# Performance work log

Measured on AMD Instinct MI355X. Metric: run time of the kernel, lower is better.

Reference implementation:

```python
import jax, jax.numpy as jnp
import numpy as np

B, S, F, H, K, NG = 256, 512, 128, 128, 8, 4
LD = H + 1  # latent_dim
EPS = 1e-12


def _ln(x, w, b):
    u = x.mean(-1, keepdims=True)
    s = ((x - u) ** 2).mean(-1, keepdims=True)
    return w * (x - u) / jnp.sqrt(s + EPS) + b


def _gru_cell(x, h, Wih, Whh, bih, bhh):
    # torch GRU gate order: reset, update, new
    gi = x @ Wih.T + bih
    gh = h @ Whh.T + bhh
    ir, iz, inn = jnp.split(gi, 3, axis=-1)
    hr, hz, hn = jnp.split(gh, 3, axis=-1)
    r = jax.nn.sigmoid(ir + hr)
    z = jax.nn.sigmoid(iz + hz)
    n = jnp.tanh(inn + r * hn)
    return (1.0 - z) * n + z * h


def setup_inputs():
    key = jax.random.key(0)
    ks = jax.random.split(key, 24)
    s = 1.0 / np.sqrt(H)
    d = {}
    d['input_data'] = jax.random.normal(ks[0], (B, S, F), jnp.float32)
    d['enc_Wih'] = jax.random.uniform(ks[1], (3 * H, F), jnp.float32, -s, s)
    d['enc_Whh'] = jax.random.uniform(ks[2], (3 * H, H), jnp.float32, -s, s)
    d['enc_bih'] = jax.random.uniform(ks[3], (3 * H,), jnp.float32, -s, s)
    d['enc_bhh'] = jax.random.uniform(ks[4], (3 * H,), jnp.float32, -s, s)
    d['dec_Wih'] = jax.random.uniform(ks[5], (3 * H, F), jnp.float32, -s, s)
    d['dec_Whh'] = jax.random.uniform(ks[6], (3 * H, H), jnp.float32, -s, s)
    d['dec_bih'] = jax.random.uniform(ks[7], (3 * H,), jnp.float32, -s, s)
    d['dec_bhh'] = jax.random.uniform(ks[8], (3 * H,), jnp.float32, -s, s)
    d['out_W'] = jax.random.uniform(ks[9], (F, H), jnp.float32, -s, s)
    d['out_b'] = jax.random.uniform(ks[10], (F,), jnp.float32, -s, s)
    d['prototypes'] = jax.random.normal(ks[11], (K, H), jnp.float32) * s
    d['lnz_w'] = jnp.ones((H,), jnp.float32)
    d['lnz_b'] = jnp.zeros((H,), jnp.float32)
    d['lnp_w'] = jnp.ones((H,), jnp.float32)
    d['lnp_b'] = jnp.zeros((H,), jnp.float32)
    d['lna_w'] = jnp.ones((H,), jnp.float32)
    d['lna_b'] = jnp.zeros((H,), jnp.float32)
    d['beta_seq'] = jax.random.normal(ks[12], (K, H), jnp.float32) * s
    d['est1_W'] = jax.random.uniform(ks[13], (10, LD), jnp.float32, -1.0 / np.sqrt(LD), 1.0 / np.sqrt(LD))
    d['est1_b'] = jax.random.uniform(ks[14], (10,), jnp.float32, -1.0 / np.sqrt(LD), 1.0 / np.sqrt(LD))
    d['est2_W'] = jax.random.uniform(ks[15], (NG, 10), jnp.float32, -1.0 / np.sqrt(10.0), 1.0 / np.sqrt(10.0))
    d['est2_b'] = jax.random.uniform(ks[16], (NG,), jnp.float32, -1.0 / np.sqrt(10.0), 1.0 / np.sqrt(10.0))
    return d


def reference(input_data, enc_Wih, enc_Whh, enc_bih, enc_bhh,
              dec_Wih, dec_Whh, dec_bih, dec_bhh, out_W, out_b,
              prototypes, lnz_w, lnz_b, lnp_w, lnp_b, lna_w, lna_b,
              beta_seq, est1_W, est1_b, est2_W, est2_b):
    bsz = input_data.shape[0]
    x_t = jnp.swapaxes(input_data, 0, 1)  # [S,B,F]

    def enc_step(h, x):
        return _gru_cell(x, h, enc_Wih, enc_Whh, enc_bih, enc_bhh), None

    h0 = jnp.zeros((bsz, H), input_data.dtype)
    h_enc, _ = jax.lax.scan(enc_step, h0, x_t)  # final hidden [B,H]

    # eval-mode decoder: emit output from hidden, then feed output back in,
    # iterating over time indices i = S-1 .. 0
    def dec_step(h, _):
        o = h @ out_W.T + out_b
        hn = _gru_cell(o, h, dec_Wih, dec_Whh, dec_bih, dec_bhh)
        return hn, o

    _, outs = jax.lax.scan(dec_step, h_enc, None, length=S)  # [S,B,F] in reversed time
    output = jnp.swapaxes(outs, 0, 1)[:, ::-1, :]  # [B,S,F]

    a = input_data.reshape(bsz, -1)
    bb = output.reshape(bsz, -1)
    na = jnp.maximum(jnp.linalg.norm(a, axis=1), 1e-8)
    nb = jnp.maximum(jnp.linalg.norm(bb, axis=1), 1e-8)
    rec_cosine = jnp.sum(a * bb, axis=1) / (na * nb)  # [B]

    # intention clustering: softmax over K prototypes
    z_ln = _ln(h_enc, lnz_w, lnz_b)            # [B,H]
    prot_ln = _ln(prototypes, lnp_w, lnp_b)    # [K,H]
    attn = jax.nn.softmax((z_ln @ prot_ln.T) / np.sqrt(H), axis=-1)  # [B,K]

    # intention aggregation: outer product [B,K,1]x[B,1,H]
    dis = beta_seq[None, :, :] + attn[:, :, None] * h_enc[:, None, :]  # [B,K,H]
    dis = _ln(dis, lna_w, lna_b)

    # resample rows per column: independent batch permutation per category
    perm_keys = jax.random.split(jax.random.key(42), K)
    perms = jnp.stack([jax.random.permutation(perm_keys[k], bsz) for k in range(K)], axis=1)  # [B,K]
    dis_perm = jnp.take_along_axis(dis, perms[:, :, None], axis=0)

    z = jnp.concatenate([dis.mean(axis=1), rec_cosine[:, None]], axis=1)  # [B,LD]
    h1 = jnp.tanh(z @ est1_W.T + est1_b)  # dropout is identity in eval
    gamma = jax.nn.softmax(h1 @ est2_W.T + est2_b, axis=1)
    return (h_enc, output, z, gamma, dis, dis_perm)
```

## Files before the change

### kernel.cpp

```cpp
#include <hip/hip_runtime.h>
#include <stdint.h>

#define Bsz 256
#define Ssz 512
#define Fsz 128
#define Hsz 128

#define HOFF_OUT   32768
#define HOFF_Z     16809984
#define HOFF_G     16843008
#define HOFF_DIS   16844032
#define HOFF_DISP  17106176

typedef __attribute__((ext_vector_type(8))) short short8;
typedef __attribute__((ext_vector_type(4))) short short4_;
typedef __attribute__((ext_vector_type(4))) float f32x4;

__device__ __forceinline__ short f2bf(float f){
  uint32_t u = __float_as_uint(f);
  u += 0x7FFFu + ((u >> 16) & 1u);
  return (short)(u >> 16);
}
__device__ __forceinline__ float bf2f(short h){
  return __uint_as_float(((uint32_t)(uint16_t)h) << 16);
}

__device__ __forceinline__ f32x4 MFMA(short8 a, short8 b, f32x4 c){
  f32x4 d;
  asm("v_mfma_f32_16x16x32_bf16 %0, %1, %2, %3" : "=v"(d) : "v"(a), "v"(b), "v"(c));
  return d;
}

__device__ __forceinline__ short8 ldcvt8(const float* p){
  float4 a = *(const float4*)p;
  float4 b = *(const float4*)(p + 4);
  short8 v;
  v[0]=f2bf(a.x); v[1]=f2bf(a.y); v[2]=f2bf(a.z); v[3]=f2bf(a.w);
  v[4]=f2bf(b.x); v[5]=f2bf(b.y); v[6]=f2bf(b.z); v[7]=f2bf(b.w);
  return v;
}
__device__ __forceinline__ void ldcvt8_2(const float* p, short8& hi, short8& lo){
  #pragma unroll
  for (int q = 0; q < 8; ++q){
    float v = p[q];
    short h = f2bf(v);
    hi[q] = h;
    lo[q] = f2bf(v - bf2f(h));
  }
}

__device__ __forceinline__ float sigm(float x){ return 1.0f/(1.0f + __expf(-x)); }
__device__ __forceinline__ float tanh_(float x){
  x = fminf(15.0f, fmaxf(-15.0f, x));
  float e = __expf(2.0f*x);
  return (e - 1.0f)/(e + 1.0f);
}

__device__ __forceinline__ int swzb(int row, int bo){ return row*256 + (bo ^ ((row & 7) << 4)); }
#define H32IDX(row, j) ((row)*128 + ((j) ^ ((((row) >> 2) & 3) << 3)))

__device__ __forceinline__ short8 ldfrag(const short* buf, int l15, int lg, int kt){
  return *(const short8*)((const char*)buf + swzb(l15, (kt*32 + lg*8)*2));
}

__device__ __forceinline__ float rsum32(float v){
  v += __shfl_xor(v,1); v += __shfl_xor(v,2); v += __shfl_xor(v,4);
  v += __shfl_xor(v,8); v += __shfl_xor(v,16); return v;
}
__device__ __forceinline__ float rsum16(float v){
  v += __shfl_xor(v,1); v += __shfl_xor(v,2); v += __shfl_xor(v,4); v += __shfl_xor(v,8);
  return v;
}

__device__ __forceinline__ void tf2x32(uint32_t k0, uint32_t k1, uint32_t x0, uint32_t x1,
                                       uint32_t& o0, uint32_t& o1){
  const uint32_t ks2 = k0 ^ k1 ^ 0x1BD11BDAu;
  uint32_t a = x0 + k0, b = x1 + k1;
#define RR(r) { a += b; b = (b << r) | (b >> (32 - r)); b ^= a; }
  RR(13) RR(15) RR(26) RR(6)   a += k1;  b += ks2 + 1u;
  RR(17) RR(29) RR(16) RR(24)  a += ks2; b += k0 + 2u;
  RR(13) RR(15) RR(26) RR(6)   a += k0;  b += k1 + 3u;
  RR(17) RR(29) RR(16) RR(24)  a += k1;  b += ks2 + 4u;
  RR(13) RR(15) RR(26) RR(6)   a += ks2; b += k0 + 5u;
#undef RR
  o0 = a; o1 = b;
}

__global__ void perm_kernel(int* __restrict__ perm){
  const int k = blockIdx.x;
  const int tid = threadIdx.x;
  __shared__ unsigned long long ck[256];
  __shared__ int nv[256];
  uint32_t pk0, pk1, sub0, sub1, o0, o1;
  tf2x32(0u, 42u, 0u, (uint32_t)k, pk0, pk1);
  tf2x32(pk0, pk1, 0u, 1u, sub0, sub1);
  tf2x32(sub0, sub1, 0u, (uint32_t)tid, o0, o1);
  const uint32_t sk = o0 ^ o1;
  unsigned long long ci = (((unsigned long long)sk) << 32) | (unsigned)tid;
  ck[tid] = ci;
  __syncthreads();
  int rank = 0;
  #pragma unroll 8
  for (int jj = 0; jj < 256; ++jj) rank += (ck[jj] < ci) ? 1 : 0;
  nv[rank] = tid;
  __syncthreads();
  perm[tid*8 + k] = nv[tid];
}

__global__ void mprep(const float* __restrict__ dWih, const float* __restrict__ dWhh,
                      const float* __restrict__ oW, const float* __restrict__ oB,
                      const float* __restrict__ dBih,
                      float* __restrict__ M, float* __restrict__ c){
  const int r = blockIdx.x;
  const int kk = threadIdx.x;
  float acc = 0.f;
  for (int f = 0; f < 128; ++f) acc += dWih[r*128 + f] * oW[f*128 + kk];
  if (r < 256) acc += dWhh[r*128 + kk];
  M[r*128 + kk] = acc;
  if (kk == 0){
    float cc = dBih[r];
    for (int f = 0; f < 128; ++f) cc += dWih[r*128 + f] * oB[f];
    c[r] = cc;
  }
}

__global__ void gatherk(const float* __restrict__ out_dis, float* __restrict__ out_disp,
                        const int* __restrict__ perm){
  int idx = blockIdx.x*512 + threadIdx.x;
  int jj = idx & 127, kk = (idx >> 7) & 7, b = idx >> 10;
  out_disp[idx] = out_dis[(perm[b*8 + kk]*8 + kk)*128 + jj];
}

__global__ __launch_bounds__(512, 2) void seqae_main(
    const float* __restrict__ x_in,
    const float* __restrict__ eWih, const float* __restrict__ eWhh,
    const float* __restrict__ eBih, const float* __restrict__ eBhh,
    const float* __restrict__ dWhh, const float* __restrict__ dBhh,
    const float* __restrict__ oW, const float* __restrict__ oB,
    const float* __restrict__ prot,
    const float* __restrict__ lnzW, const float* __restrict__ lnzB,
    const float* __restrict__ lnpW, const float* __restrict__ lnpB,
    const float* __restrict__ lnaW, const float* __restrict__ lnaB,
    const float* __restrict__ beta,
    const float* __restrict__ e1W, const float* __restrict__ e1B,
    const float* __restrict__ e2W, const float* __restrict__ e2B,
    const float* __restrict__ Mws, const float* __restrict__ cws,
    float* __restrict__ out)
{
  __shared__ short hbuf[2][2048];
  __shared__ short hlob[2][2048];
  __shared__ short xbuf[2][2048];
  __shared__ float h32[2][2048];
  __shared__ float henc[2048];

  const int tid = threadIdx.x;
  const int w = tid >> 6, lane = tid & 63;
  const int l15 = lane & 15, lg = lane >> 4;
  const int bbase = blockIdx.x * 16;
  const int jrow = w*16 + l15;
  const int srow = tid >> 5, schunk = tid & 31;
  const int j = jrow;

  const float be_r  = eBih[j]       + eBhh[j];
  const float be_z  = eBih[128 + j] + eBhh[128 + j];
  const float be_in = eBih[256 + j];
  const float be_hn = eBhh[256 + j];
  const float bd_r  = cws[j]        + dBhh[j];
  const float bd_z  = cws[128 + j]  + dBhh[128 + j];
  const float bd_in = cws[256 + j];
  const float bd_hn = dBhh[256 + j];
  const float b_o   = oB[j];

  for (int i = tid; i < 2048; i += 512){ h32[0][i] = 0.f; hbuf[0][i] = 0; hlob[0][i] = 0; }

  short8 ex_r[4], ex_z[4], ex_i[4];
  short8 eh_rh[4], eh_rl[4], eh_zh[4], eh_zl[4], eh_nh[4], eh_nl[4];
  #pragma unroll
  for (int kt = 0; kt < 4; ++kt){
    const int off = kt*32 + lg*8;
    ex_r[kt] = ldcvt8(eWih + (      j)*128 + off);
    ex_z[kt] = ldcvt8(eWih + (128 + j)*128 + off);
    ex_i[kt] = ldcvt8(eWih + (256 + j)*128 + off);
    ldcvt8_2(eWhh + (      j)*128 + off, eh_rh[kt], eh_rl[kt]);
    ldcvt8_2(eWhh + (128 + j)*128 + off, eh_zh[kt], eh_zl[kt]);
    ldcvt8_2(eWhh + (256 + j)*128 + off, eh_nh[kt], eh_nl[kt]);
  }

  float na_reg = 0.f;
  {
    float4 xf = *(const float4*)(x_in + ((bbase + srow)*Ssz + 0)*Fsz + schunk*4);
    na_reg += xf.x*xf.x + xf.y*xf.y + xf.z*xf.z + xf.w*xf.w;
    short4_ s; s[0]=f2bf(xf.x); s[1]=f2bf(xf.y); s[2]=f2bf(xf.z); s[3]=f2bf(xf.w);
    *(short4_*)((char*)&xbuf[0][0] + swzb(srow, schunk*8)) = s;
  }
  __syncthreads();

  for (int t = 0; t < Ssz; ++t){
    const int cur = t & 1, nxt = cur ^ 1;
    float4 xf;
    const bool hav = (t + 1 < Ssz);
    if (hav) xf = *(const float4*)(x_in + ((bbase + srow)*Ssz + (t+1))*Fsz + schunk*4);

    short8 axf[4], ahh[4], ahl[4];
    #pragma unroll
    for (int kt = 0; kt < 4; ++kt){
      axf[kt] = ldfrag(&xbuf[cur][0], l15, lg, kt);
      ahh[kt] = ldfrag(&hbuf[cur][0], l15, lg, kt);
      ahl[kt] = ldfrag(&hlob[cur][0], l15, lg, kt);
    }
    f32x4 ar = {0,0,0,0}, az = {0,0,0,0}, ai = {0,0,0,0}, an = {0,0,0,0};
    #pragma unroll
    for (int kt = 0; kt < 4; ++kt){
      ar = MFMA(axf[kt], ex_r[kt], ar);
      az = MFMA(axf[kt], ex_z[kt], az);
      ai = MFMA(axf[kt], ex_i[kt], ai);
      ar = MFMA(ahh[kt], eh_rh[kt], ar);
      ar = MFMA(ahl[kt], eh_rh[kt], ar);
      ar = MFMA(ahh[kt], eh_rl[kt], ar);
      az = MFMA(ahh[kt], eh_zh[kt], az);
      az = MFMA(ahl[kt], eh_zh[kt], az);
      az = MFMA(ahh[kt], eh_zl[kt], az);
      an = MFMA(ahh[kt], eh_nh[kt], an);
      an = MFMA(ahl[kt], eh_nh[kt], an);
      an = MFMA(ahh[kt], eh_nl[kt], an);
    }
    #pragma unroll
    for (int reg = 0; reg < 4; ++reg){
      const int row = lg*4 + reg;
      float r = sigm(ar[reg] + be_r);
      float z = sigm(az[reg] + be_z);
      float n = tanh_(ai[reg] + be_in + r*(an[reg] + be_hn));
      float hold = h32[cur][H32IDX(row, j)];
      float hv = n + z*(hold - n);
      h32[nxt][H32IDX(row, j)] = hv;
      short hh = f2bf(hv);
      short hl = f2bf(hv - bf2f(hh));
      *(short*)((char*)&hbuf[nxt][0] + swzb(row, 2*j)) = hh;
      *(short*)((char*)&hlob[nxt][0] + swzb(row, 2*j)) = hl;
    }
    if (hav){
      na_reg += xf.x*xf.x + xf.y*xf.y + xf.z*xf.z + xf.w*xf.w;
      short4_ s; s[0]=f2bf(xf.x); s[1]=f2bf(xf.y); s[2]=f2bf(xf.z); s[3]=f2bf(xf.w);
      *(short4_*)((char*)&xbuf[nxt][0] + swzb(srow, schunk*8)) = s;
    }
    __syncthreads();
  }

  for (int i2 = tid; i2 < 2048; i2 += 512){
    int row = i2 >> 7, jj = i2 & 127;
    float v = h32[0][H32IDX(row, jj)];
    henc[i2] = v;
    out[(bbase + row)*128 + jj] = v;
  }

  short8 d_oh[4], d_ol[4], d_rh[4], d_rl[4], d_zh[4], d_zl[4], d_ih[4], d_il[4], d_nh[4], d_nl[4];
  #pragma unroll
  for (int kt = 0; kt < 4; ++kt){
    const int off = kt*32 + lg*8;
    ldcvt8_2(oW   + (      j)*128 + off, d_oh[kt], d_ol[kt]);
    ldcvt8_2(Mws  + (      j)*128 + off, d_rh[kt], d_rl[kt]);
    ldcvt8_2(Mws  + (128 + j)*128 + off, d_zh[kt], d_zl[kt]);
    ldcvt8_2(Mws  + (256 + j)*128 + off, d_ih[kt], d_il[kt]);
    ldcvt8_2(dWhh + (256 + j)*128 + off, d_nh[kt], d_nl[kt]);
  }

  float dot_p[4] = {0,0,0,0}, nb_p[4] = {0,0,0,0};
  for (int i = 0; i < Ssz; ++i){
    const int cur = i & 1, nxt = cur ^ 1;
    const int tt = Ssz - 1 - i;
    float xv[4];
    #pragma unroll
    for (int reg = 0; reg < 4; ++reg){
      const int row = lg*4 + reg;
      xv[reg] = x_in[((bbase + row)*Ssz + tt)*Fsz + j];
    }
    short8 ahh[4], ahl[4];
    #pragma unroll
    for (int kt = 0; kt < 4; ++kt){
      ahh[kt] = ldfrag(&hbuf[cur][0], l15, lg, kt);
      ahl[kt] = ldfrag(&hlob[cur][0], l15, lg, kt);
    }
    f32x4 ao = {0,0,0,0}, ar = {0,0,0,0}, az = {0,0,0,0}, ai = {0,0,0,0}, an = {0,0,0,0};
    #pragma unroll
    for (int kt = 0; kt < 4; ++kt){
      ao = MFMA(ahh[kt], d_oh[kt], ao);
      ao = MFMA(ahl[kt], d_oh[kt], ao);
      ao = MFMA(ahh[kt], d_ol[kt], ao);
      ar = MFMA(ahh[kt], d_rh[kt], ar);
      ar = MFMA(ahl[kt], d_rh[kt], ar);
      ar = MFMA(ahh[kt], d_rl[kt], ar);
      az = MFMA(ahh[kt], d_zh[kt], az);
      az = MFMA(ahl[kt], d_zh[kt], az);
      az = MFMA(ahh[kt], d_zl[kt], az);
      ai = MFMA(ahh[kt], d_ih[kt], ai);
      ai = MFMA(ahl[kt], d_ih[kt], ai);
      ai = MFMA(ahh[kt], d_il[kt], ai);
      an = MFMA(ahh[kt], d_nh[kt], an);
      an = MFMA(ahl[kt], d_nh[kt], an);
      an = MFMA(ahh[kt], d_nl[kt], an);
    }
    #pragma unroll
    for (int reg = 0; reg < 4; ++reg){
      const int row = lg*4 + reg;
      float o = ao[reg] + b_o;
      float r = sigm(ar[reg] + bd_r);
      float z = sigm(az[reg] + bd_z);
      float n = tanh_(ai[reg] + bd_in + r*(an[reg] + bd_hn));
      float hold = h32[cur][H32IDX(row, j)];
      float hv = n + z*(hold - n);
      h32[nxt][H32IDX(row, j)] = hv;
      short hh = f2bf(hv);
      short hl = f2bf(hv - bf2f(hh));
      *(short*)((char*)&hbuf[nxt][0] + swzb(row, 2*j)) = hh;
      *(short*)((char*)&hlob[nxt][0] + swzb(row, 2*j)) = hl;
      out[HOFF_OUT + ((bbase + row)*Ssz + tt)*Fsz + j] = o;
      dot_p[reg] += xv[reg]*o;
      nb_p[reg]  += o*o;
    }
    __syncthreads();
  }

  float (*s_zln)[128] = reinterpret_cast<float(*)[128]>(&xbuf[0][0]);
  float (*s_pln)[128] = reinterpret_cast<float(*)[128]>(&h32[0][0]);
  float (*s_att)[8]   = reinterpret_cast<float(*)[8]>(&h32[0][1024]);
  float (*s_h1)[10]   = reinterpret_cast<float(*)[10]>(&h32[0][1152]);
  float (*red)[8][16] = reinterpret_cast<float(*)[8][16]>(&h32[1][0]);
  float *s_na = &h32[1][256];
  float *s_rc = &h32[1][272];

  {
    float v = rsum32(na_reg);
    if ((tid & 31) == 0) s_na[srow] = v;
  }
  #pragma unroll
  for (int reg = 0; reg < 4; ++reg){
    float d  = rsum16(dot_p[reg]);
    float nb = rsum16(nb_p[reg]);
    if (l15 == 0){ red[0][w][lg*4 + reg] = d; red[1][w][lg*4 + reg] = nb; }
  }
  __syncthreads();
  if (tid < 16){
    float d = 0.f, nb = 0.f;
    #pragma unroll
    for (int ww = 0; ww < 8; ++ww){ d += red[0][ww][tid]; nb += red[1][ww][tid]; }
    s_rc[tid] = d / (fmaxf(sqrtf(s_na[tid]), 1e-8f) * fmaxf(sqrtf(nb), 1e-8f));
  }

  {
    const int rr = srow, tl = schunk;
    float xv4[4]; float sm = 0.f, sq = 0.f;
    #pragma unroll
    for (int q = 0; q < 4; ++q){ float v = henc[rr*128 + q*32 + tl]; xv4[q] = v; sm += v; sq += v*v; }
    sm = rsum32(sm); sq = rsum32(sq);
    float u = sm*(1.f/128.f), var = sq*(1.f/128.f) - u*u;
    float inv = rsqrtf(var + 1e-12f);
    #pragma unroll
    for (int q = 0; q < 4; ++q){ int jj = q*32 + tl; s_zln[rr][jj] = lnzW[jj]*(xv4[q]-u)*inv + lnzB[jj]; }
  }
  if (tid < 256){
    const int pr = tid >> 5, tl = tid & 31;
    float xv4[4]; float sm = 0.f, sq = 0.f;
    #pragma unroll
    for (int q = 0; q < 4; ++q){ float v = prot[pr*128 + q*32 + tl]; xv4[q] = v; sm += v; sq += v*v; }
    sm = rsum32(sm); sq = rsum32(sq);
    float u = sm*(1.f/128.f), var = sq*(1.f/128.f) - u*u;
    float inv = rsqrtf(var + 1e-12f);
    #pragma unroll
    for (int q = 0; q < 4; ++q){ int jj = q*32 + tl; s_pln[pr][jj] = lnpW[jj]*(xv4[q]-u)*inv + lnpB[jj]; }
  }
  __syncthreads();

  {
    const int gid = tid >> 2, tq = tid & 3;
    const int rr2 = gid >> 3, kk = gid & 7;
    float p = 0.f;
    #pragma unroll 8
    for (int q = 0; q < 32; ++q){ int jj = tq + 4*q; p += s_zln[rr2][jj]*s_pln[kk][jj]; }
    p += __shfl_xor(p, 1); p += __shfl_xor(p, 2);
    if (tq == 0) s_att[rr2][kk] = p * 0.08838834764831845f;
  }
  __syncthreads();
  if (tid < 16){
    float mx = -1e30f;
    #pragma unroll
    for (int kk = 0; kk < 8; ++kk) mx = fmaxf(mx, s_att[tid][kk]);
    float sum = 0.f; float e[8];
    #pragma unroll
    for (int kk = 0; kk < 8; ++kk){ e[kk] = __expf(s_att[tid][kk] - mx); sum += e[kk]; }
    #pragma unroll
    for (int kk = 0; kk < 8; ++kk) s_att[tid][kk] = e[kk]/sum;
  }
  __syncthreads();

  {
    const int rr = srow, tl = schunk;
    float dmq[4] = {0,0,0,0};
    for (int kk = 0; kk < 8; ++kk){
      float a = s_att[rr][kk];
      float vv[4]; float sm = 0.f, sq = 0.f;
      #pragma unroll
      for (int q = 0; q < 4; ++q){
        int jj = q*32 + tl;
        float v = beta[kk*128 + jj] + a*henc[rr*128 + jj];
        vv[q] = v; sm += v; sq += v*v;
      }
      sm = rsum32(sm); sq = rsum32(sq);
      float u = sm*(1.f/128.f), var = sq*(1.f/128.f) - u*u;
      float inv = rsqrtf(var + 1e-12f);
      #pragma unroll
      for (int q = 0; q < 4; ++q){
        int jj = q*32 + tl;
        float dv = lnaW[jj]*(vv[q]-u)*inv + lnaB[jj];
        out[HOFF_DIS + ((bbase + rr)*8 + kk)*128 + jj] = dv;
        dmq[q] += dv;
      }
    }
    #pragma unroll
    for (int q = 0; q < 4; ++q){
      int jj = q*32 + tl;
      float dm = dmq[q]*0.125f;
      out[HOFF_Z + (bbase + rr)*129 + jj] = dm;
      s_zln[rr][jj] = dm;
    }
    if (tl == 0) out[HOFF_Z + (bbase + rr)*129 + 128] = s_rc[rr];
  }
  __syncthreads();

  if (tid < 160){
    const int rr = tid/10, ii = tid%10;
    float acc = e1B[ii];
    const float* wrow = e1W + ii*129;
    for (int dd = 0; dd < 128; ++dd) acc += wrow[dd]*s_zln[rr][dd];
    acc += wrow[128]*s_rc[rr];
    s_h1[rr][ii] = tanh_(acc);
  }
  __syncthreads();
  if (tid < 16){
    float g[4]; float mx = -1e30f;
    #pragma unroll
    for (int ii = 0; ii < 4; ++ii){
      float a = e2B[ii];
      #pragma unroll
      for (int dd = 0; dd < 10; ++dd) a += e2W[ii*10 + dd]*s_h1[tid][dd];
      g[ii] = a; mx = fmaxf(mx, a);
    }
    float sum = 0.f;
    #pragma unroll
    for (int ii = 0; ii < 4; ++ii){ g[ii] = __expf(g[ii] - mx); sum += g[ii]; }
    #pragma unroll
    for (int ii = 0; ii < 4; ++ii) out[HOFF_G + (bbase + tid)*4 + ii] = g[ii]/sum;
  }
}

extern "C" void kernel_launch(void* const* d_in, const int* in_sizes, int n_in,
                              void* d_out, int out_size, void* d_ws, size_t ws_size,
                              hipStream_t stream){
  (void)in_sizes; (void)n_in; (void)out_size; (void)ws_size;
  const float* x    = (const float*)d_in[0];
  const float* eWih = (const float*)d_in[1];
  const float* eWhh = (const float*)d_in[2];
  const float* eBih = (const float*)d_in[3];
  const float* eBhh = (const float*)d_in[4];
  const float* dWih = (const float*)d_in[5];
  const float* dWhh = (const float*)d_in[6];
  const float* dBih = (const float*)d_in[7];
  const float* dBhh = (const float*)d_in[8];
  const float* oW   = (const float*)d_in[9];
  const float* oB   = (const float*)d_in[10];
  const float* prot = (const float*)d_in[11];
  const float* lnzW = (const float*)d_in[12];
  const float* lnzB = (const float*)d_in[13];
  const float* lnpW = (const float*)d_in[14];
  const float* lnpB = (const float*)d_in[15];
  const float* lnaW = (const float*)d_in[16];
  const float* lnaB = (const float*)d_in[17];
  const float* beta = (const float*)d_in[18];
  const float* e1W  = (const float*)d_in[19];
  const float* e1B  = (const float*)d_in[20];
  const float* e2W  = (const float*)d_in[21];
  const float* e2B  = (const float*)d_in[22];

  float* Mws = (float*)d_ws;
  float* cws = Mws + 384*128;
  int*  perm = (int*)(cws + 384);
  float* out = (float*)d_out;

  hipLaunchKernelGGL(mprep, dim3(384), dim3(128), 0, stream, dWih, dWhh, oW, oB, dBih, Mws, cws);
  hipLaunchKernelGGL(perm_kernel, dim3(8), dim3(256), 0, stream, perm);
  hipLaunchKernelGGL(seqae_main, dim3(16), dim3(512), 0, stream,
      x, eWih, eWhh, eBih, eBhh, dWhh, dBhh, oW, oB, prot,
      lnzW, lnzB, lnpW, lnpB, lnaW, lnaB, beta, e1W, e1B, e2W, e2B, Mws, cws, out);
  hipLaunchKernelGGL(gatherk, dim3(512), dim3(512), 0, stream, out + HOFF_DIS, out + HOFF_DISP, perm);
}
```

Before: 2.124 ms.

## Keep GRU state in registers, split MFMA chains, unroll steps with light barriers

```diff
diff --git a/kernel.cpp b/kernel.cpp
--- a/kernel.cpp
+++ b/kernel.cpp
@@ -13,7 +13,6 @@
 #define HOFF_DISP  17106176
 
 typedef __attribute__((ext_vector_type(8))) short short8;
-typedef __attribute__((ext_vector_type(4))) short short4_;
 typedef __attribute__((ext_vector_type(4))) float f32x4;
 
 __device__ __forceinline__ short f2bf(float f){
@@ -32,11 +31,9 @@
 }
 
 __device__ __forceinline__ short8 ldcvt8(const float* p){
-  float4 a = *(const float4*)p;
-  float4 b = *(const float4*)(p + 4);
   short8 v;
-  v[0]=f2bf(a.x); v[1]=f2bf(a.y); v[2]=f2bf(a.z); v[3]=f2bf(a.w);
-  v[4]=f2bf(b.x); v[5]=f2bf(b.y); v[6]=f2bf(b.z); v[7]=f2bf(b.w);
+  #pragma unroll
+  for (int q = 0; q < 8; ++q) v[q] = f2bf(p[q]);
   return v;
 }
 __device__ __forceinline__ void ldcvt8_2(const float* p, short8& hi, short8& lo){
@@ -56,11 +53,10 @@
   return (e - 1.0f)/(e + 1.0f);
 }
 
-__device__ __forceinline__ int swzb(int row, int bo){ return row*256 + (bo ^ ((row & 7) << 4)); }
-#define H32IDX(row, j) ((row)*128 + ((j) ^ ((((row) >> 2) & 3) << 3)))
-
-__device__ __forceinline__ short8 ldfrag(const short* buf, int l15, int lg, int kt){
-  return *(const short8*)((const char*)buf + swzb(l15, (kt*32 + lg*8)*2));
+__device__ __forceinline__ void lbar(){
+  asm volatile("s_waitcnt lgkmcnt(0)" ::: "memory");
+  __builtin_amdgcn_s_barrier();
+  asm volatile("" ::: "memory");
 }
 
 __device__ __forceinline__ float rsum32(float v){
@@ -130,6 +126,8 @@
   int jj = idx & 127, kk = (idx >> 7) & 7, b = idx >> 10;
   out_disp[idx] = out_dis[(perm[b*8 + kk]*8 + kk)*128 + jj];
 }
+
+#define FRAG(base, off) (*(const short8*)((const char*)(base) + (off)))
 
 __global__ __launch_bounds__(512, 2) void seqae_main(
     const float* __restrict__ x_in,
@@ -147,19 +145,17 @@
     const float* __restrict__ Mws, const float* __restrict__ cws,
     float* __restrict__ out)
 {
-  __shared__ short hbuf[2][2048];
-  __shared__ short hlob[2][2048];
-  __shared__ short xbuf[2][2048];
-  __shared__ float h32[2][2048];
-  __shared__ float henc[2048];
+  __shared__ __align__(16) short hbuf[2][2048];
+  __shared__ __align__(16) short hlob[2][2048];
+  __shared__ __align__(16) short xbuf[2][2048];
+  __shared__ __align__(16) float henc[2048];
 
   const int tid = threadIdx.x;
   const int w = tid >> 6, lane = tid & 63;
   const int l15 = lane & 15, lg = lane >> 4;
   const int bbase = blockIdx.x * 16;
-  const int jrow = w*16 + l15;
+  const int j = w*16 + l15;
   const int srow = tid >> 5, schunk = tid & 31;
-  const int j = jrow;
 
   const float be_r  = eBih[j]       + eBhh[j];
   const float be_z  = eBih[128 + j] + eBhh[128 + j];
@@ -171,7 +167,20 @@
   const float bd_hn = dBhh[256 + j];
   const float b_o   = oB[j];
 
-  for (int i = tid; i < 2048; i += 512){ h32[0][i] = 0.f; hbuf[0][i] = 0; hlob[0][i] = 0; }
+  int fo[4];
+  #pragma unroll
+  for (int kt = 0; kt < 4; ++kt)
+    fo[kt] = l15*256 + ((kt*64 + lg*16) ^ ((l15 & 7) << 4));
+  int wo[4];
+  #pragma unroll
+  for (int reg = 0; reg < 4; ++reg){
+    int row = lg*4 + reg;
+    wo[reg] = row*256 + ((2*j) ^ ((row & 7) << 4));
+  }
+  const int xwo = srow*256 + ((schunk*8) ^ ((srow & 7) << 4));
+
+  for (int i = tid; i < 2048; i += 512){ hbuf[0][i] = 0; hlob[0][i] = 0; }
+  float hold[4] = {0.f, 0.f, 0.f, 0.f};
 
   short8 ex_r[4], ex_z[4], ex_i[4];
   short8 eh_rh[4], eh_rl[4], eh_zh[4], eh_zl[4], eh_nh[4], eh_nl[4];
@@ -186,71 +195,99 @@
     ldcvt8_2(eWhh + (256 + j)*128 + off, eh_nh[kt], eh_nl[kt]);
   }
 
+#define STORE_H(NXT, hv) do { \
+    uint32_t pkh0, pkh1, pkl0, pkl1; \
+    asm("v_cvt_pk_bf16_f32 %0, %1, %2" : "=v"(pkh0) : "v"(hv[0]), "v"(hv[1])); \
+    asm("v_cvt_pk_bf16_f32 %0, %1, %2" : "=v"(pkh1) : "v"(hv[2]), "v"(hv[3])); \
+    float l0 = hv[0] - __uint_as_float(pkh0 << 16); \
+    float l1 = hv[1] - __uint_as_float(pkh0 & 0xffff0000u); \
+    float l2 = hv[2] - __uint_as_float(pkh1 << 16); \
+    float l3 = hv[3] - __uint_as_float(pkh1 & 0xffff0000u); \
+    asm("v_cvt_pk_bf16_f32 %0, %1, %2" : "=v"(pkl0) : "v"(l0), "v"(l1)); \
+    asm("v_cvt_pk_bf16_f32 %0, %1, %2" : "=v"(pkl1) : "v"(l2), "v"(l3)); \
+    char* hbp = (char*)&hbuf[NXT][0]; char* lbp = (char*)&hlob[NXT][0]; \
+    *(short*)(hbp + wo[0]) = (short)(pkh0); \
+    *(short*)(hbp + wo[1]) = (short)(pkh0 >> 16); \
+    *(short*)(hbp + wo[2]) = (short)(pkh1); \
+    *(short*)(hbp + wo[3]) = (short)(pkh1 >> 16); \
+    *(short*)(lbp + wo[0]) = (short)(pkl0); \
+    *(short*)(lbp + wo[1]) = (short)(pkl0 >> 16); \
+    *(short*)(lbp + wo[2]) = (short)(pkl1); \
+    *(short*)(lbp + wo[3]) = (short)(pkl1 >> 16); \
+  } while(0)
+
+#define XSTAGE(NXT, xf) do { \
+    na_reg += xf.x*xf.x + xf.y*xf.y + xf.z*xf.z + xf.w*xf.w; \
+    uint32_t p0, p1; \
+    asm("v_cvt_pk_bf16_f32 %0, %1, %2" : "=v"(p0) : "v"(xf.x), "v"(xf.y)); \
+    asm("v_cvt_pk_bf16_f32 %0, %1, %2" : "=v"(p1) : "v"(xf.z), "v"(xf.w)); \
+    *(uint64_t*)((char*)&xbuf[NXT][0] + xwo) = ((uint64_t)p1 << 32) | p0; \
+  } while(0)
+
+#define ENC_STEP(CUR) do { \
+    short8 axf[4], ahh[4], ahl[4]; \
+    _Pragma("unroll") \
+    for (int kt = 0; kt < 4; ++kt){ \
+      axf[kt] = FRAG(&xbuf[CUR][0], fo[kt]); \
+      ahh[kt] = FRAG(&hbuf[CUR][0], fo[kt]); \
+      ahl[kt] = FRAG(&hlob[CUR][0], fo[kt]); \
+    } \
+    f32x4 arA={0,0,0,0}, arB={0,0,0,0}, azA={0,0,0,0}, azB={0,0,0,0}; \
+    f32x4 anA={0,0,0,0}, anB={0,0,0,0}, ai4={0,0,0,0}; \
+    _Pragma("unroll") \
+    for (int kt = 0; kt < 4; ++kt){ \
+      arA = MFMA(axf[kt], ex_r[kt], arA); \
+      azA = MFMA(axf[kt], ex_z[kt], azA); \
+      anA = MFMA(ahh[kt], eh_nh[kt], anA); \
+      ai4 = MFMA(axf[kt], ex_i[kt], ai4); \
+      arB = MFMA(ahh[kt], eh_rh[kt], arB); \
+      azB = MFMA(ahh[kt], eh_zh[kt], azB); \
+      anB = MFMA(ahl[kt], eh_nh[kt], anB); \
+      arA = MFMA(ahl[kt], eh_rh[kt], arA); \
+      azA = MFMA(ahl[kt], eh_zh[kt], azA); \
+      anA = MFMA(ahh[kt], eh_nl[kt], anA); \
+      arB = MFMA(ahh[kt], eh_rl[kt], arB); \
+      azB = MFMA(ahh[kt], eh_zl[kt], azB); \
+    } \
+    f32x4 arS = arA + arB, azS = azA + azB, anS = anA + anB; \
+    float hv[4]; \
+    _Pragma("unroll") \
+    for (int reg = 0; reg < 4; ++reg){ \
+      float r = sigm(arS[reg] + be_r); \
+      float z = sigm(azS[reg] + be_z); \
+      float n = tanh_(ai4[reg] + be_in + r*(anS[reg] + be_hn)); \
+      float h2 = n + z*(hold[reg] - n); \
+      hold[reg] = h2; hv[reg] = h2; \
+    } \
+    STORE_H(CUR ^ 1, hv); \
+  } while(0)
+
   float na_reg = 0.f;
+  const int xoff_lane = ((bbase + srow)*Ssz)*Fsz + schunk*4;
   {
-    float4 xf = *(const float4*)(x_in + ((bbase + srow)*Ssz + 0)*Fsz + schunk*4);
-    na_reg += xf.x*xf.x + xf.y*xf.y + xf.z*xf.z + xf.w*xf.w;
-    short4_ s; s[0]=f2bf(xf.x); s[1]=f2bf(xf.y); s[2]=f2bf(xf.z); s[3]=f2bf(xf.w);
-    *(short4_*)((char*)&xbuf[0][0] + swzb(srow, schunk*8)) = s;
-  }
-  __syncthreads();
-
-  for (int t = 0; t < Ssz; ++t){
-    const int cur = t & 1, nxt = cur ^ 1;
-    float4 xf;
-    const bool hav = (t + 1 < Ssz);
-    if (hav) xf = *(const float4*)(x_in + ((bbase + srow)*Ssz + (t+1))*Fsz + schunk*4);
-
-    short8 axf[4], ahh[4], ahl[4];
-    #pragma unroll
-    for (int kt = 0; kt < 4; ++kt){
-      axf[kt] = ldfrag(&xbuf[cur][0], l15, lg, kt);
-      ahh[kt] = ldfrag(&hbuf[cur][0], l15, lg, kt);
-      ahl[kt] = ldfrag(&hlob[cur][0], l15, lg, kt);
-    }
-    f32x4 ar = {0,0,0,0}, az = {0,0,0,0}, ai = {0,0,0,0}, an = {0,0,0,0};
-    #pragma unroll
-    for (int kt = 0; kt < 4; ++kt){
-      ar = MFMA(axf[kt], ex_r[kt], ar);
-      az = MFMA(axf[kt], ex_z[kt], az);
-      ai = MFMA(axf[kt], ex_i[kt], ai);
-      ar = MFMA(ahh[kt], eh_rh[kt], ar);
-      ar = MFMA(ahl[kt], eh_rh[kt], ar);
-      ar = MFMA(ahh[kt], eh_rl[kt], ar);
-      az = MFMA(ahh[kt], eh_zh[kt], az);
-      az = MFMA(ahl[kt], eh_zh[kt], az);
-      az = MFMA(ahh[kt], eh_zl[kt], az);
-      an = MFMA(ahh[kt], eh_nh[kt], an);
-      an = MFMA(ahl[kt], eh_nh[kt], an);
-      an = MFMA(ahh[kt], eh_nl[kt], an);
-    }
-    #pragma unroll
-    for (int reg = 0; reg < 4; ++reg){
-      const int row = lg*4 + reg;
-      float r = sigm(ar[reg] + be_r);
-      float z = sigm(az[reg] + be_z);
-      float n = tanh_(ai[reg] + be_in + r*(an[reg] + be_hn));
-      float hold = h32[cur][H32IDX(row, j)];
-      float hv = n + z*(hold - n);
-      h32[nxt][H32IDX(row, j)] = hv;
-      short hh = f2bf(hv);
-      short hl = f2bf(hv - bf2f(hh));
-      *(short*)((char*)&hbuf[nxt][0] + swzb(row, 2*j)) = hh;
-      *(short*)((char*)&hlob[nxt][0] + swzb(row, 2*j)) = hl;
-    }
-    if (hav){
-      na_reg += xf.x*xf.x + xf.y*xf.y + xf.z*xf.z + xf.w*xf.w;
-      short4_ s; s[0]=f2bf(xf.x); s[1]=f2bf(xf.y); s[2]=f2bf(xf.z); s[3]=f2bf(xf.w);
-      *(short4_*)((char*)&xbuf[nxt][0] + swzb(srow, schunk*8)) = s;
-    }
-    __syncthreads();
-  }
-
-  for (int i2 = tid; i2 < 2048; i2 += 512){
-    int row = i2 >> 7, jj = i2 & 127;
-    float v = h32[0][H32IDX(row, jj)];
-    henc[i2] = v;
-    out[(bbase + row)*128 + jj] = v;
+    float4 xf = *(const float4*)(x_in + xoff_lane);
+    XSTAGE(0, xf);
+  }
+  __syncthreads();
+
+  for (int t = 0; t < Ssz; t += 2){
+    float4 xf1 = *(const float4*)(x_in + xoff_lane + (t+1)*Fsz);
+    ENC_STEP(0);
+    XSTAGE(1, xf1);
+    lbar();
+    const bool hav2 = (t + 2 < Ssz);
+    float4 xf2;
+    if (hav2) xf2 = *(const float4*)(x_in + xoff_lane + (t+2)*Fsz);
+    ENC_STEP(1);
+    if (hav2) XSTAGE(0, xf2);
+    lbar();
+  }
+
+  #pragma unroll
+  for (int reg = 0; reg < 4; ++reg){
+    int row = lg*4 + reg;
+    henc[row*128 + j] = hold[reg];
+    out[(bbase + row)*128 + j] = hold[reg];
   }
 
   short8 d_oh[4], d_ol[4], d_rh[4], d_rl[4], d_zh[4], d_zl[4], d_ih[4], d_il[4], d_nh[4], d_nl[4];
@@ -263,70 +300,82 @@
     ldcvt8_2(Mws  + (256 + j)*128 + off, d_ih[kt], d_il[kt]);
     ldcvt8_2(dWhh + (256 + j)*128 + off, d_nh[kt], d_nl[kt]);
   }
+  (void)d_ol;
+
+  int doff[4];
+  #pragma unroll
+  for (int reg = 0; reg < 4; ++reg){
+    int row = lg*4 + reg;
+    doff[reg] = (bbase + row)*Ssz*Fsz + j;
+  }
 
   float dot_p[4] = {0,0,0,0}, nb_p[4] = {0,0,0,0};
-  for (int i = 0; i < Ssz; ++i){
-    const int cur = i & 1, nxt = cur ^ 1;
+
+#define DEC_STEP(CUR, TT) do { \
+    const float* xt = x_in + (size_t)(TT)*Fsz; \
+    float* ot = out + HOFF_OUT + (size_t)(TT)*Fsz; \
+    float xv[4]; \
+    _Pragma("unroll") \
+    for (int reg = 0; reg < 4; ++reg) xv[reg] = xt[doff[reg]]; \
+    short8 ahh[4], ahl[4]; \
+    _Pragma("unroll") \
+    for (int kt = 0; kt < 4; ++kt){ \
+      ahh[kt] = FRAG(&hbuf[CUR][0], fo[kt]); \
+      ahl[kt] = FRAG(&hlob[CUR][0], fo[kt]); \
+    } \
+    f32x4 ao4={0,0,0,0}, arA={0,0,0,0}, arB={0,0,0,0}, azA={0,0,0,0}, azB={0,0,0,0}; \
+    f32x4 aiA={0,0,0,0}, aiB={0,0,0,0}, anA={0,0,0,0}, anB={0,0,0,0}; \
+    _Pragma("unroll") \
+    for (int kt = 0; kt < 4; ++kt){ \
+      ao4 = MFMA(ahh[kt], d_oh[kt], ao4); \
+      arA = MFMA(ahh[kt], d_rh[kt], arA); \
+      azA = MFMA(ahh[kt], d_zh[kt], azA); \
+      aiA = MFMA(ahh[kt], d_ih[kt], aiA); \
+      anA = MFMA(ahh[kt], d_nh[kt], anA); \
+      arB = MFMA(ahl[kt], d_rh[kt], arB); \
+      azB = MFMA(ahl[kt], d_zh[kt], azB); \
+      aiB = MFMA(ahl[kt], d_ih[kt], aiB); \
+      anB = MFMA(ahl[kt], d_nh[kt], anB); \
+      arB = MFMA(ahh[kt], d_rl[kt], arB); \
+      azB = MFMA(ahh[kt], d_zl[kt], azB); \
+      aiB = MFMA(ahh[kt], d_il[kt], aiB); \
+      anB = MFMA(ahh[kt], d_nl[kt], anB); \
+    } \
+    f32x4 arS = arA + arB, azS = azA + azB, aiS = aiA + aiB, anS = anA + anB; \
+    float hv[4], ov[4]; \
+    _Pragma("unroll") \
+    for (int reg = 0; reg < 4; ++reg){ \
+      float o = ao4[reg] + b_o; \
+      float r = sigm(arS[reg] + bd_r); \
+      float z = sigm(azS[reg] + bd_z); \
+      float n = tanh_(aiS[reg] + bd_in + r*(anS[reg] + bd_hn)); \
+      float h2 = n + z*(hold[reg] - n); \
+      hold[reg] = h2; hv[reg] = h2; ov[reg] = o; \
+    } \
+    STORE_H(CUR ^ 1, hv); \
+    _Pragma("unroll") \
+    for (int reg = 0; reg < 4; ++reg){ \
+      ot[doff[reg]] = ov[reg]; \
+      dot_p[reg] += xv[reg]*ov[reg]; \
+      nb_p[reg]  += ov[reg]*ov[reg]; \
+    } \
+    lbar(); \
+  } while(0)
+
+  for (int i = 0; i < Ssz; i += 2){
     const int tt = Ssz - 1 - i;
-    float xv[4];
-    #pragma unroll
-    for (int reg = 0; reg < 4; ++reg){
-      const int row = lg*4 + reg;
-      xv[reg] = x_in[((bbase + row)*Ssz + tt)*Fsz + j];
-    }
-    short8 ahh[4], ahl[4];
-    #pragma unroll
-    for (int kt = 0; kt < 4; ++kt){
-      ahh[kt] = ldfrag(&hbuf[cur][0], l15, lg, kt);
-      ahl[kt] = ldfrag(&hlob[cur][0], l15, lg, kt);
-    }
-    f32x4 ao = {0,0,0,0}, ar = {0,0,0,0}, az = {0,0,0,0}, ai = {0,0,0,0}, an = {0,0,0,0};
-    #pragma unroll
-    for (int kt = 0; kt < 4; ++kt){
-      ao = MFMA(ahh[kt], d_oh[kt], ao);
-      ao = MFMA(ahl[kt], d_oh[kt], ao);
-      ao = MFMA(ahh[kt], d_ol[kt], ao);
-      ar = MFMA(ahh[kt], d_rh[kt], ar);
-      ar = MFMA(ahl[kt], d_rh[kt], ar);
-      ar = MFMA(ahh[kt], d_rl[kt], ar);
-      az = MFMA(ahh[kt], d_zh[kt], az);
-      az = MFMA(ahl[kt], d_zh[kt], az);
-      az = MFMA(ahh[kt], d_zl[kt], az);
-      ai = MFMA(ahh[kt], d_ih[kt], ai);
-      ai = MFMA(ahl[kt], d_ih[kt], ai);
-      ai = MFMA(ahh[kt], d_il[kt], ai);
-      an = MFMA(ahh[kt], d_nh[kt], an);
-      an = MFMA(ahl[kt], d_nh[kt], an);
-      an = MFMA(ahh[kt], d_nl[kt], an);
-    }
-    #pragma unroll
-    for (int reg = 0; reg < 4; ++reg){
-      const int row = lg*4 + reg;
-      float o = ao[reg] + b_o;
-      float r = sigm(ar[reg] + bd_r);
-      float z = sigm(az[reg] + bd_z);
-      float n = tanh_(ai[reg] + bd_in + r*(an[reg] + bd_hn));
-      float hold = h32[cur][H32IDX(row, j)];
-      float hv = n + z*(hold - n);
-      h32[nxt][H32IDX(row, j)] = hv;
-      short hh = f2bf(hv);
-      short hl = f2bf(hv - bf2f(hh));
-      *(short*)((char*)&hbuf[nxt][0] + swzb(row, 2*j)) = hh;
-      *(short*)((char*)&hlob[nxt][0] + swzb(row, 2*j)) = hl;
-      out[HOFF_OUT + ((bbase + row)*Ssz + tt)*Fsz + j] = o;
-      dot_p[reg] += xv[reg]*o;
-      nb_p[reg]  += o*o;
-    }
-    __syncthreads();
+    DEC_STEP(0, tt);
+    DEC_STEP(1, tt - 1);
   }
 
   float (*s_zln)[128] = reinterpret_cast<float(*)[128]>(&xbuf[0][0]);
-  float (*s_pln)[128] = reinterpret_cast<float(*)[128]>(&h32[0][0]);
-  float (*s_att)[8]   = reinterpret_cast<float(*)[8]>(&h32[0][1024]);
-  float (*s_h1)[10]   = reinterpret_cast<float(*)[10]>(&h32[0][1152]);
-  float (*red)[8][16] = reinterpret_cast<float(*)[8][16]>(&h32[1][0]);
-  float *s_na = &h32[1][256];
-  float *s_rc = &h32[1][272];
+  float (*s_pln)[128] = reinterpret_cast<float(*)[128]>(&hbuf[0][0]);
+  float* lf = reinterpret_cast<float*>(&hlob[0][0]);
+  float (*red)[8][16] = reinterpret_cast<float(*)[8][16]>(lf);
+  float* s_na = lf + 256;
+  float* s_rc = lf + 272;
+  float (*s_att)[8]   = reinterpret_cast<float(*)[8]>(lf + 288);
+  float (*s_h1)[10]   = reinterpret_cast<float(*)[10]>(lf + 416);
 
   {
     float v = rsum32(na_reg);
```

New measurement: 2.025 ms. -4.6%, faster.
